# Optimization experiments

Measured on AMD Instinct MI355X. Metric: run time of the kernel, lower is better.

The kernel has to match this reference:

```python
import jax, jax.numpy as jnp
import numpy as np

B, S, D_IN, D_OUT = 4, 4096, 256, 256

def setup_inputs() -> dict:
    key = jax.random.key(0)
    ks = jax.random.split(key, 7)
    scale = 1.0 / np.sqrt(D_IN)
    return {
        "x": jax.random.normal(ks[0], (B, S, D_IN), dtype=jnp.float32),
        "Wq": jax.random.uniform(ks[1], (D_IN, D_OUT), jnp.float32, -scale, scale),
        "bq": jax.random.uniform(ks[2], (D_OUT,), jnp.float32, -scale, scale),
        "Wk": jax.random.uniform(ks[3], (D_IN, D_OUT), jnp.float32, -scale, scale),
        "bk": jax.random.uniform(ks[4], (D_OUT,), jnp.float32, -scale, scale),
        "Wv": jax.random.uniform(ks[5], (D_IN, D_OUT), jnp.float32, -scale, scale),
        "bv": jax.random.uniform(ks[6], (D_OUT,), jnp.float32, -scale, scale),
    }

def reference(x, Wq, bq, Wk, bk, Wv, bv):
    # QKV projections: [B, S, D_OUT]
    q = jnp.einsum("bsd,de->bse", x, Wq) + bq
    k = jnp.einsum("bsd,de->bse", x, Wk) + bk
    v = jnp.einsum("bsd,de->bse", x, Wv) + bv
    # Scaled dot-product attention; full [B, S, S] scores as in the original.
    scores = jnp.einsum("bqe,bke->bqk", q, k) / jnp.sqrt(jnp.asarray(q.shape[-1], q.dtype))
    attn = jax.nn.softmax(scores, axis=-1)
    return jnp.einsum("bqk,bke->bqe", attn, v)
```

## Files before the change

kernel.cpp:

```cpp
#include <hip/hip_runtime.h>
#include <stdint.h>

typedef unsigned short u16;
typedef __attribute__((ext_vector_type(4))) float f32x4;
typedef __attribute__((ext_vector_type(8))) short bf16x8;
typedef __attribute__((ext_vector_type(4))) int i32x4;
typedef __attribute__((ext_vector_type(2))) unsigned int u32x2;

#define SEQ 4096
#define DIM 256
#define QSCALE 0.09016844f

__device__ __forceinline__ u16 f2bf(float f) {
  union { float f; uint32_t u; } v; v.f = f;
  uint32_t r = (v.u + 0x7FFFu + ((v.u >> 16) & 1u)) >> 16;
  return (u16)r;
}

__device__ __forceinline__ void gload_lds16(const void* g, void* lds) {
  __builtin_amdgcn_global_load_lds(
      (const __attribute__((address_space(1))) uint32_t*)g,
      (__attribute__((address_space(3))) uint32_t*)lds, 16, 0, 0);
}

__global__ __launch_bounds__(256) void wt_kernel(const float* __restrict__ Wq,
                                                 const float* __restrict__ Wk,
                                                 const float* __restrict__ Wv,
                                                 u16* __restrict__ wt) {
  int b = blockIdx.x;
  int w = b >> 8;
  int n = b & 255;
  const float* W = (w == 0) ? Wq : ((w == 1) ? Wk : Wv);
  float scale = (w == 0) ? QSCALE : 1.0f;
  int k = threadIdx.x;
  wt[(w * 256 + n) * 256 + k] = f2bf(W[k * 256 + n] * scale);
}

__global__ __launch_bounds__(256) void qkv_kernel(
    const float* __restrict__ x, const float* __restrict__ bq,
    const float* __restrict__ bk, const float* __restrict__ bv,
    const u16* __restrict__ wt, u16* __restrict__ qs, u16* __restrict__ kk,
    char* __restrict__ vt) {
  __shared__ __align__(16) u16 lds_b[16384];
  __shared__ __align__(16) u16 lds_v[4096];
  int tid = threadIdx.x;
  int w = tid >> 6, l = tid & 63;
  int a = l & 15, g = l >> 4;
  int rowbase = blockIdx.x * 64;

  bf16x8 afr[8];
  {
    int row = rowbase + w * 16 + a;
    const float* xr = x + (size_t)row * 256;
#pragma unroll
    for (int ks = 0; ks < 8; ++ks) {
      int k0 = ks * 32 + g * 8;
      union { bf16x8 s; u16 u[8]; } fr;
#pragma unroll
      for (int i = 0; i < 8; ++i) fr.u[i] = f2bf(xr[k0 + i]);
      afr[ks] = fr.s;
    }
  }

  for (int w3 = 0; w3 < 3; ++w3) {
    const float* bias = (w3 == 0) ? bq : ((w3 == 1) ? bk : bv);
    for (int qn = 0; qn < 4; ++qn) {
      {
        const u16* src = wt + (w3 * 256 + qn * 64) * 256;
        for (int j = 0; j < 8; ++j) {
          uint32_t inst = w * 8 + j;
          uint32_t flat = inst * 1024 + l * 16;
          uint32_t row = flat >> 9;
          uint32_t c5 = (flat >> 4) & 31;
          uint32_t sc = (c5 & ~7u) | ((c5 ^ row) & 7u);
          gload_lds16(src + row * 256 + sc * 8, ((char*)lds_b) + inst * 1024);
        }
      }
      __syncthreads();
      f32x4 acc[4];
#pragma unroll
      for (int n0 = 0; n0 < 4; ++n0) acc[n0] = (f32x4){0.f, 0.f, 0.f, 0.f};
#pragma unroll
      for (int ks = 0; ks < 8; ++ks) {
#pragma unroll
        for (int n0 = 0; n0 < 4; ++n0) {
          uint32_t row = n0 * 16 + a;
          uint32_t c5 = ks * 4 + g;
          uint32_t sc = (c5 & ~7u) | ((c5 ^ row) & 7u);
          bf16x8 bfr = *(const bf16x8*)((const char*)lds_b + row * 512 + sc * 16);
          acc[n0] = __builtin_amdgcn_mfma_f32_16x16x32_bf16(afr[ks], bfr, acc[n0], 0, 0, 0);
        }
      }
      if (w3 < 2) {
        u16* out = (w3 == 0) ? qs : kk;
        float bscale = (w3 == 0) ? QSCALE : 1.0f;
#pragma unroll
        for (int n0 = 0; n0 < 4; ++n0) {
          int col = qn * 64 + n0 * 16 + a;
          float bb = bias[col] * bscale;
#pragma unroll
          for (int r = 0; r < 4; ++r) {
            int row = rowbase + w * 16 + g * 4 + r;
            out[(size_t)row * 256 + col] = f2bf(acc[n0][r] + bb);
          }
        }
      } else {
#pragma unroll
        for (int n0 = 0; n0 < 4; ++n0) {
          int col = qn * 64 + n0 * 16 + a;
          float bb = bias[col];
          int dl = n0 * 16 + a;
#pragma unroll
          for (int r = 0; r < 4; ++r) {
            int m = w * 16 + g * 4 + r;
            uint32_t byteoff =
                (uint32_t)dl * 128 + ((((uint32_t)m >> 3) ^ ((uint32_t)dl & 7)) << 4) + (m & 7) * 2;
            *(u16*)((char*)lds_v + byteoff) = f2bf(acc[n0][r] + bb);
          }
        }
        __syncthreads();
        {
          int dl = tid >> 2;
          size_t base = (size_t)blockIdx.x * 32768 + (size_t)(qn * 64 + dl) * 128;
#pragma unroll
          for (int cc = 0; cc < 2; ++cc) {
            uint32_t c = (tid & 3) + cc * 4;
            i32x4 vd = *(const i32x4*)((const char*)lds_v + dl * 128 + ((c ^ (dl & 7)) << 4));
            *(i32x4*)(vt + base + c * 16) = vd;
          }
        }
      }
      __syncthreads();
    }
  }
}

__device__ __forceinline__ void stage4(const char* src, char* ldsbase,
                                       const uint32_t* so, int w) {
#pragma unroll
  for (int j = 0; j < 4; ++j)
    gload_lds16(src + so[j], ldsbase + (w * 4 + j) * 1024);
}

#define PV_STEP(SLOT)                                                          \
  {                                                                            \
    bf16x8 pfr[2][2];                                                          \
    _Pragma("unroll") for (int mt = 0; mt < 2; ++mt)                           \
    _Pragma("unroll") for (int j2 = 0; j2 < 2; ++j2)                           \
        pfr[mt][j2] = *(const bf16x8*)(lds + (SLOT) * 16384 + pro[j2] + mt * 2048); \
    __builtin_amdgcn_s_setprio(1);                                             \
    _Pragma("unroll") for (int mt = 0; mt < 2; ++mt)                           \
    _Pragma("unroll") for (int j2 = 0; j2 < 2; ++j2)                           \
        lacc[mt] = __builtin_amdgcn_mfma_f32_16x16x32_bf16(pfr[mt][j2], ones,  \
                                                           lacc[mt], 0, 0, 0); \
    _Pragma("unroll") for (int d0 = 0; d0 < 8; ++d0)                           \
    _Pragma("unroll") for (int j2 = 0; j2 < 2; ++j2) {                         \
      bf16x8 vfr = *(const bf16x8*)(lds + 65536 + (SLOT) * 32768 + vro[j2] +   \
                                    d0 * 2048);                                \
      o[0][d0] = __builtin_amdgcn_mfma_f32_16x16x32_bf16(pfr[0][j2], vfr, o[0][d0], 0, 0, 0); \
      o[1][d0] = __builtin_amdgcn_mfma_f32_16x16x32_bf16(pfr[1][j2], vfr, o[1][d0], 0, 0, 0); \
    }                                                                          \
    __builtin_amdgcn_s_setprio(0);                                             \
  }

#define TILE(CUR, DO_PV, DO_K)                                                 \
  {                                                                            \
    asm volatile("s_waitcnt vmcnt(0) lgkmcnt(0)" ::: "memory");                \
    __builtin_amdgcn_s_barrier();                                              \
    __builtin_amdgcn_sched_barrier(0);                                         \
    stage4(vstp, lds + 65536 + (CUR) * 32768, vso, w);   \
    if (DO_K) stage4(kstp, lds + ((CUR) ^ 1) * 32768, kso, w);  \
    kstp += 32768;                                                             \
    vstp += 32768;                                                             \
    f32x4 sc[2][2];                                                            \
    _Pragma("unroll") for (int mt = 0; mt < 2; ++mt)                           \
    _Pragma("unroll") for (int n = 0; n < 2; ++n)                              \
        sc[mt][n] = (f32x4){0.f, 0.f, 0.f, 0.f};                               \
    __builtin_amdgcn_s_setprio(1);                                             \
    _Pragma("unroll") for (int n = 0; n < 2; ++n)                              \
    _Pragma("unroll") for (int j = 0; j < 8; ++j) {                            \
      bf16x8 kfr = *(const bf16x8*)(lds + (CUR) * 32768 + kro[j] + n * 8192);  \
      sc[0][n] = __builtin_amdgcn_mfma_f32_16x16x32_bf16(kfr, qfr[0][j], sc[0][n], 0, 0, 0); \
      sc[1][n] = __builtin_amdgcn_mfma_f32_16x16x32_bf16(kfr, qfr[1][j], sc[1][n], 0, 0, 0); \
    }                                                                          \
    __builtin_amdgcn_s_setprio(0);                                             \
    _Pragma("unroll") for (int mt = 0; mt < 2; ++mt)                           \
    _Pragma("unroll") for (int n = 0; n < 2; ++n) {                            \
      float e0 = exp2f(fminf(sc[mt][n][0], 43.f));                             \
      float e1 = exp2f(fminf(sc[mt][n][1], 43.f));                             \
      float e2 = exp2f(fminf(sc[mt][n][2], 43.f));                             \
      float e3 = exp2f(fminf(sc[mt][n][3], 43.f));                             \
      uint32_t p0 = (uint32_t)f2bf(e0) | ((uint32_t)f2bf(e1) << 16);           \
      uint32_t p1 = (uint32_t)f2bf(e2) | ((uint32_t)f2bf(e3) << 16);           \
      u32x2 pk = {p0, p1};                                                     \
      *(u32x2*)(lds + (CUR) * 16384 + pwo[n] + mt * 2048) = pk;                \
    }                                                                          \
    if (DO_PV) PV_STEP((CUR) ^ 1)                                              \
  }

__global__ __launch_bounds__(512, 1) void attn_kernel(
    const u16* __restrict__ qs, const u16* __restrict__ kk,
    const char* __restrict__ vt, float* __restrict__ out,
    float* __restrict__ pOB, float* __restrict__ pl, int split) {
  __shared__ __align__(16) char lds[163840];
  int tid = threadIdx.x;
  int w = tid >> 6, l = tid & 63;
  int a = l & 15, g = l >> 4;
  int qq = w >> 1, sub = w & 1;
  int bx = blockIdx.x;
  int h, batch, qt;
  if (split == 2) { h = bx & 1; batch = (bx >> 1) & 3; qt = bx >> 3; }
  else            { h = 0;      batch = (bx >> 1) & 3; qt = ((bx >> 3) << 1) | (bx & 1); }
  int ntHalf = (split == 2) ? 16 : 32;

  uint32_t a7 = a & 7;
  uint32_t kro[8], vro[2], pro[2], pwo[2], kso[4], vso[4];
#pragma unroll
  for (int j = 0; j < 8; ++j) {
    uint32_t c5 = j * 4 + g;
    kro[j] = (uint32_t)(sub * 32 + a) * 512 +
             (((c5 & ~7u) | ((c5 ^ a7) & 7u)) << 4);
  }
#pragma unroll
  for (int j2 = 0; j2 < 2; ++j2)
    vro[j2] = (uint32_t)(sub * 128 + a) * 128 +
              ((((uint32_t)(j2 * 4 + g)) ^ a7) << 4);
#pragma unroll
  for (int j2 = 0; j2 < 2; ++j2)
    pro[j2] = 131072u + (uint32_t)(qq * 32 + a) * 128 +
              ((((uint32_t)(j2 * 4 + g)) ^ a7) << 4);
#pragma unroll
  for (int n = 0; n < 2; ++n)
    pwo[n] = 131072u + (uint32_t)(qq * 32 + a) * 128 +
             ((((uint32_t)(sub * 4 + n * 2 + (g >> 1))) ^ a7) << 4) + (g & 1) * 8;
#pragma unroll
  for (int j = 0; j < 4; ++j) {
    uint32_t inst = w * 4 + j, flat = inst * 1024 + l * 16;
    {
      uint32_t row = flat >> 9, c5 = (flat >> 4) & 31;
      kso[j] = row * 512 + (((c5 & ~7u) | ((c5 ^ row) & 7u)) << 4);
    }
    {
      uint32_t row = flat >> 7, c3 = (flat >> 4) & 7;
      vso[j] = row * 128 + ((c3 ^ (row & 7)) << 4);
    }
  }

  bf16x8 qfr[2][8];
  {
    const char* qp = (const char*)qs + (size_t)(batch * SEQ + qt * 128) * 512;
#pragma unroll
    for (int mt = 0; mt < 2; ++mt)
#pragma unroll
      for (int j = 0; j < 8; ++j)
        qfr[mt][j] = *(const bf16x8*)(qp + (size_t)(qq * 32 + mt * 16 + a) * 512 +
                                      j * 64 + g * 16);
  }

  f32x4 o[2][8];
  f32x4 lacc[2];
#pragma unroll
  for (int mt = 0; mt < 2; ++mt) {
    lacc[mt] = (f32x4){0.f, 0.f, 0.f, 0.f};
#pragma unroll
    for (int d0 = 0; d0 < 8; ++d0) o[mt][d0] = (f32x4){0.f, 0.f, 0.f, 0.f};
  }
  const short ob = (short)0x3F80;
  bf16x8 ones = {ob, ob, ob, ob, ob, ob, ob, ob};

  const char* kstp = (const char*)kk + (size_t)batch * SEQ * 512 + (size_t)h * 2048 * 512;
  const char* vstp = vt + (size_t)batch * 64 * 32768 + (size_t)h * 32 * 32768;

  stage4(kstp, lds, kso, w);
  kstp += 32768;

  TILE(0, false, true)
  for (int tp = 0; tp < ntHalf - 1; ++tp) {
    TILE(1, true, true)
    TILE(0, true, true)
  }
  TILE(1, true, false)

  asm volatile("s_waitcnt vmcnt(0) lgkmcnt(0)" ::: "memory");
  __builtin_amdgcn_s_barrier();
  __builtin_amdgcn_sched_barrier(0);
  PV_STEP(1)

  float* po = (h == 0) ? out : pOB;
  size_t obase = (size_t)(batch * SEQ + qt * 128 + qq * 32) * 256 + sub * 128;
#pragma unroll
  for (int mt = 0; mt < 2; ++mt)
#pragma unroll
    for (int r = 0; r < 4; ++r) {
#pragma unroll
      for (int d0 = 0; d0 < 8; ++d0)
        po[obase + (size_t)(mt * 16 + g * 4 + r) * 256 + d0 * 16 + a] = o[mt][d0][r];
    }
  if (a == 0 && sub == 0) {
#pragma unroll
    for (int mt = 0; mt < 2; ++mt)
#pragma unroll
      for (int r = 0; r < 4; ++r)
        pl[h * 16384 + (batch * 32 + qt) * 128 + qq * 32 + mt * 16 + g * 4 + r] =
            lacc[mt][r];
  }
}

__global__ __launch_bounds__(256) void combine_kernel(float* __restrict__ out,
                                                      const float* __restrict__ pOB,
                                                      const float* __restrict__ pl,
                                                      int split) {
  int b = blockIdx.x;
  int tid = threadIdx.x;
  int batch = b >> 12;
  int rem = b & 4095;
  int qt = rem >> 7, ql = rem & 127;
  size_t idx = (size_t)b * 256 + tid;
  int li = (batch * 32 + qt) * 128 + ql;
  float lA = pl[li];
  float v;
  if (split == 2) {
    float lB = pl[16384 + li];
    v = (out[idx] + pOB[idx]) / (lA + lB);
  } else {
    v = out[idx] / lA;
  }
  out[idx] = v;
}

extern "C" void kernel_launch(void* const* d_in, const int* in_sizes, int n_in,
                              void* d_out, int out_size, void* d_ws, size_t ws_size,
                              hipStream_t stream) {
  const float* x = (const float*)d_in[0];
  const float* Wq = (const float*)d_in[1];
  const float* bq = (const float*)d_in[2];
  const float* Wk = (const float*)d_in[3];
  const float* bk = (const float*)d_in[4];
  const float* Wv = (const float*)d_in[5];
  const float* bv = (const float*)d_in[6];
  char* ws = (char*)d_ws;
  u16* wt = (u16*)ws;
  u16* qs = (u16*)(ws + 0x60000);
  u16* kk = (u16*)(ws + 0x860000);
  char* vt = ws + 0x1060000;
  float* pl = (float*)(ws + 0x1860000);
  float* pOB = (float*)(ws + 0x1880000);
  int split = (ws_size >= 0x2880000ull) ? 2 : 1;
  wt_kernel<<<dim3(768), dim3(256), 0, stream>>>(Wq, Wk, Wv, wt);
  qkv_kernel<<<dim3(256), dim3(256), 0, stream>>>(x, bq, bk, bv, wt, qs, kk, vt);
  attn_kernel<<<dim3(split * 128), dim3(512), 0, stream>>>(qs, kk, vt, (float*)d_out,
                                                           pOB, pl, split);
  combine_kernel<<<dim3(16384), dim3(256), 0, stream>>>((float*)d_out, pOB, pl, split);
}
```

Measured before the change: 129.1 us.

## Add 4-way key-split attention kernel with single-buffered LDS staging

Adds an attn4_kernel that splits the key dimension into four chunks, launching 512 blocks instead of 256 so more CUs are busy. Each block handles 1024 keys in 16 tiles and writes partial outputs and row sums to workspace. The combine kernel now sums up to four partials. The new kernel drops the double-buffered K/V prefetch and waits on each load, and it adds extra partial-output traffic. It is only used when the workspace is large enough.

```diff
diff --git a/kernel.cpp b/kernel.cpp
--- a/kernel.cpp
+++ b/kernel.cpp
@@ -168,8 +168,8 @@
     asm volatile("s_waitcnt vmcnt(0) lgkmcnt(0)" ::: "memory");                \
     __builtin_amdgcn_s_barrier();                                              \
     __builtin_amdgcn_sched_barrier(0);                                         \
-    stage4(vstp, lds + 65536 + (CUR) * 32768, vso, w);   \
-    if (DO_K) stage4(kstp, lds + ((CUR) ^ 1) * 32768, kso, w);  \
+    stage4(vstp, lds + 65536 + (CUR) * 32768, vso, w);                         \
+    if (DO_K) stage4(kstp, lds + ((CUR) ^ 1) * 32768, kso, w);                 \
     kstp += 32768;                                                             \
     vstp += 32768;                                                             \
     f32x4 sc[2][2];                                                            \
@@ -306,6 +306,169 @@
   }
 }
 
+__global__ __launch_bounds__(512, 4) void attn4_kernel(
+    const u16* __restrict__ qs, const u16* __restrict__ kk,
+    const char* __restrict__ vt, float* __restrict__ out,
+    float* __restrict__ pOB, float* __restrict__ pl) {
+  __shared__ __align__(16) char lds[81920];
+  int tid = threadIdx.x;
+  int w = tid >> 6, l = tid & 63;
+  int a = l & 15, g = l >> 4;
+  int qq = w >> 1, sub = w & 1;
+  int bx = blockIdx.x;
+  int xcd = bx & 7, slot = bx >> 3;
+  int combo = xcd * 2 + (slot >> 5);
+  int batch = combo >> 2, h = combo & 3;
+  int qt = slot & 31;
+
+  uint32_t a7 = a & 7;
+  uint32_t kro[8], vro[2], pro[2], pwo[2], kso[4], vso[4];
+#pragma unroll
+  for (int j = 0; j < 8; ++j) {
+    uint32_t c5 = j * 4 + g;
+    kro[j] = (uint32_t)(sub * 32 + a) * 512 +
+             (((c5 & ~7u) | ((c5 ^ a7) & 7u)) << 4);
+  }
+#pragma unroll
+  for (int j2 = 0; j2 < 2; ++j2)
+    vro[j2] = 32768u + (uint32_t)(sub * 128 + a) * 128 +
+              ((((uint32_t)(j2 * 4 + g)) ^ a7) << 4);
+#pragma unroll
+  for (int j2 = 0; j2 < 2; ++j2)
+    pro[j2] = 65536u + (uint32_t)(qq * 32 + a) * 128 +
+              ((((uint32_t)(j2 * 4 + g)) ^ a7) << 4);
+#pragma unroll
+  for (int n = 0; n < 2; ++n)
+    pwo[n] = 65536u + (uint32_t)(qq * 32 + a) * 128 +
+             ((((uint32_t)(sub * 4 + n * 2 + (g >> 1))) ^ a7) << 4) + (g & 1) * 8;
+#pragma unroll
+  for (int j = 0; j < 4; ++j) {
+    uint32_t inst = w * 4 + j, flat = inst * 1024 + l * 16;
+    {
+      uint32_t row = flat >> 9, c5 = (flat >> 4) & 31;
+      kso[j] = row * 512 + (((c5 & ~7u) | ((c5 ^ row) & 7u)) << 4);
+    }
+    {
+      uint32_t row = flat >> 7, c3 = (flat >> 4) & 7;
+      vso[j] = row * 128 + ((c3 ^ (row & 7)) << 4);
+    }
+  }
+
+  bf16x8 qfr[2][8];
+  {
+    const char* qp = (const char*)qs + (size_t)(batch * SEQ + qt * 128) * 512;
+#pragma unroll
+    for (int mt = 0; mt < 2; ++mt)
+#pragma unroll
+      for (int j = 0; j < 8; ++j)
+        qfr[mt][j] = *(const bf16x8*)(qp + (size_t)(qq * 32 + mt * 16 + a) * 512 +
+                                      j * 64 + g * 16);
+  }
+
+  f32x4 o[2][8];
+  f32x4 lacc[2];
+#pragma unroll
+  for (int mt = 0; mt < 2; ++mt) {
+    lacc[mt] = (f32x4){0.f, 0.f, 0.f, 0.f};
+#pragma unroll
+    for (int d0 = 0; d0 < 8; ++d0) o[mt][d0] = (f32x4){0.f, 0.f, 0.f, 0.f};
+  }
+  const short ob = (short)0x3F80;
+  bf16x8 ones = {ob, ob, ob, ob, ob, ob, ob, ob};
+
+  const char* kstp = (const char*)kk + (size_t)batch * SEQ * 512 + (size_t)h * 1024 * 512;
+  const char* vstp = vt + (size_t)batch * 64 * 32768 + (size_t)h * 16 * 32768;
+
+  for (int t = 0; t < 16; ++t) {
+    stage4(kstp, lds, kso, w);
+    stage4(vstp, lds + 32768, vso, w);
+    kstp += 32768;
+    vstp += 32768;
+    asm volatile("s_waitcnt vmcnt(0)" ::: "memory");
+    __builtin_amdgcn_s_barrier();
+    __builtin_amdgcn_sched_barrier(0);
+
+    f32x4 sc[2][2];
+#pragma unroll
+    for (int mt = 0; mt < 2; ++mt)
+#pragma unroll
+      for (int n = 0; n < 2; ++n) sc[mt][n] = (f32x4){0.f, 0.f, 0.f, 0.f};
+    __builtin_amdgcn_s_setprio(1);
+#pragma unroll
+    for (int n = 0; n < 2; ++n)
+#pragma unroll
+      for (int j = 0; j < 8; ++j) {
+        bf16x8 kfr = *(const bf16x8*)(lds + kro[j] + n * 8192);
+        sc[0][n] = __builtin_amdgcn_mfma_f32_16x16x32_bf16(kfr, qfr[0][j], sc[0][n], 0, 0, 0);
+        sc[1][n] = __builtin_amdgcn_mfma_f32_16x16x32_bf16(kfr, qfr[1][j], sc[1][n], 0, 0, 0);
+      }
+    __builtin_amdgcn_s_setprio(0);
+
+#pragma unroll
+    for (int mt = 0; mt < 2; ++mt)
+#pragma unroll
+      for (int n = 0; n < 2; ++n) {
+        float e0 = exp2f(fminf(sc[mt][n][0], 43.f));
+        float e1 = exp2f(fminf(sc[mt][n][1], 43.f));
+        float e2 = exp2f(fminf(sc[mt][n][2], 43.f));
+        float e3 = exp2f(fminf(sc[mt][n][3], 43.f));
+        uint32_t p0 = (uint32_t)f2bf(e0) | ((uint32_t)f2bf(e1) << 16);
+        uint32_t p1 = (uint32_t)f2bf(e2) | ((uint32_t)f2bf(e3) << 16);
+        u32x2 pk = {p0, p1};
+        *(u32x2*)(lds + pwo[n] + mt * 2048) = pk;
+      }
+    asm volatile("s_waitcnt lgkmcnt(0)" ::: "memory");
+    __builtin_amdgcn_s_barrier();
+    __builtin_amdgcn_sched_barrier(0);
+
+    {
+      bf16x8 pfr[2][2];
+#pragma unroll
+      for (int mt = 0; mt < 2; ++mt)
+#pragma unroll
+        for (int j2 = 0; j2 < 2; ++j2)
+          pfr[mt][j2] = *(const bf16x8*)(lds + pro[j2] + mt * 2048);
+      __builtin_amdgcn_s_setprio(1);
+#pragma unroll
+      for (int mt = 0; mt < 2; ++mt)
+#pragma unroll
+        for (int j2 = 0; j2 < 2; ++j2)
+          lacc[mt] = __builtin_amdgcn_mfma_f32_16x16x32_bf16(pfr[mt][j2], ones,
+                                                             lacc[mt], 0, 0, 0);
+#pragma unroll
+      for (int d0 = 0; d0 < 8; ++d0)
+#pragma unroll
+        for (int j2 = 0; j2 < 2; ++j2) {
+          bf16x8 vfr = *(const bf16x8*)(lds + vro[j2] + d0 * 2048);
+          o[0][d0] = __builtin_amdgcn_mfma_f32_16x16x32_bf16(pfr[0][j2], vfr, o[0][d0], 0, 0, 0);
+          o[1][d0] = __builtin_amdgcn_mfma_f32_16x16x32_bf16(pfr[1][j2], vfr, o[1][d0], 0, 0, 0);
+        }
+      __builtin_amdgcn_s_setprio(0);
+    }
+    __builtin_amdgcn_s_barrier();
+    __builtin_amdgcn_sched_barrier(0);
+  }
+
+  float* po = (h == 0) ? out : (pOB + (size_t)(h - 1) * 0x400000);
+  size_t obase = (size_t)(batch * SEQ + qt * 128 + qq * 32) * 256 + sub * 128;
+#pragma unroll
+  for (int mt = 0; mt < 2; ++mt)
+#pragma unroll
+    for (int r = 0; r < 4; ++r) {
+#pragma unroll
+      for (int d0 = 0; d0 < 8; ++d0)
+        po[obase + (size_t)(mt * 16 + g * 4 + r) * 256 + d0 * 16 + a] = o[mt][d0][r];
+    }
+  if (a == 0 && sub == 0) {
+#pragma unroll
+    for (int mt = 0; mt < 2; ++mt)
+#pragma unroll
+      for (int r = 0; r < 4; ++r)
+        pl[h * 16384 + (batch * 32 + qt) * 128 + qq * 32 + mt * 16 + g * 4 + r] =
+            lacc[mt][r];
+  }
+}
+
 __global__ __launch_bounds__(256) void combine_kernel(float* __restrict__ out,
                                                       const float* __restrict__ pOB,
                                                       const float* __restrict__ pl,
@@ -317,15 +480,14 @@
   int qt = rem >> 7, ql = rem & 127;
   size_t idx = (size_t)b * 256 + tid;
   int li = (batch * 32 + qt) * 128 + ql;
-  float lA = pl[li];
-  float v;
-  if (split == 2) {
-    float lB = pl[16384 + li];
-    v = (out[idx] + pOB[idx]) / (lA + lB);
-  } else {
-    v = out[idx] / lA;
-  }
-  out[idx] = v;
+  float lsum = pl[li];
+  float v = out[idx];
+  if (split >= 2) { lsum += pl[16384 + li]; v += pOB[idx]; }
+  if (split == 4) {
+    lsum += pl[32768 + li] + pl[49152 + li];
+    v += pOB[idx + 0x400000] + pOB[idx + 0x800000];
+  }
+  out[idx] = v / lsum;
 }
 
 extern "C" void kernel_launch(void* const* d_in, const int* in_sizes, int n_in,
@@ -344,11 +506,21 @@
   u16* kk = (u16*)(ws + 0x860000);
   char* vt = ws + 0x1060000;
   float* pl = (float*)(ws + 0x1860000);
-  float* pOB = (float*)(ws + 0x1880000);
-  int split = (ws_size >= 0x2880000ull) ? 2 : 1;
+  float* pOB2 = (float*)(ws + 0x1880000);
+  float* pOB4 = (float*)(ws + 0x18A0000);
+  int split;
+  if (ws_size >= 0x48A0000ull) split = 4;
+  else if (ws_size >= 0x2880000ull) split = 2;
+  else split = 1;
   wt_kernel<<<dim3(768), dim3(256), 0, stream>>>(Wq, Wk, Wv, wt);
   qkv_kernel<<<dim3(256), dim3(256), 0, stream>>>(x, bq, bk, bv, wt, qs, kk, vt);
-  attn_kernel<<<dim3(split * 128), dim3(512), 0, stream>>>(qs, kk, vt, (float*)d_out,
-                                                           pOB, pl, split);
-  combine_kernel<<<dim3(16384), dim3(256), 0, stream>>>((float*)d_out, pOB, pl, split);
-}
+  if (split == 4) {
+    attn4_kernel<<<dim3(512), dim3(512), 0, stream>>>(qs, kk, vt, (float*)d_out,
+                                                      pOB4, pl);
+    combine_kernel<<<dim3(16384), dim3(256), 0, stream>>>((float*)d_out, pOB4, pl, 4);
+  } else {
+    attn_kernel<<<dim3(split * 128), dim3(512), 0, stream>>>(qs, kk, vt, (float*)d_out,
+                                                             pOB2, pl, split);
+    combine_kernel<<<dim3(16384), dim3(256), 0, stream>>>((float*)d_out, pOB2, pl, split);
+  }
+}
```

Result: slower. 477.2 us (+269.6%).

## Use FP8 Q/K for scores, enlarge query tile to 256, split KV four ways

Applied to the files above, without the earlier changes.

Q and K projections are now stored as FP8 (with Q scaled by 4x the softmax factor and K by 0.25 so the range fits FP8), and QK^T uses the fp8 MFMA, halving K staging bytes and LDS footprint. Each attention block now handles 256 query rows instead of 128, which raises reuse of each staged K/V tile, and the KV sequence is split across 4 blocks instead of 2, with XCD-aware block mapping. The combine kernel sums four partial outputs and denominators. FP8 scores reduce accuracy, and the larger register tile (o[4][8]) raises register pressure.

```diff
diff --git a/kernel.cpp b/kernel.cpp
--- a/kernel.cpp
+++ b/kernel.cpp
@@ -2,6 +2,7 @@
 #include <stdint.h>
 
 typedef unsigned short u16;
+typedef long long i64;
 typedef __attribute__((ext_vector_type(4))) float f32x4;
 typedef __attribute__((ext_vector_type(8))) short bf16x8;
 typedef __attribute__((ext_vector_type(4))) int i32x4;
@@ -10,6 +11,7 @@
 #define SEQ 4096
 #define DIM 256
 #define QSCALE 0.09016844f
+#define QS4 0.36067376f
 
 __device__ __forceinline__ u16 f2bf(float f) {
   union { float f; uint32_t u; } v; v.f = f;
@@ -17,10 +19,18 @@
   return (u16)r;
 }
 
+__device__ __forceinline__ uint8_t f2fp8(float f) {
+  return (uint8_t)__builtin_amdgcn_cvt_pk_fp8_f32(f, 0.f, 0, false);
+}
+
 __device__ __forceinline__ void gload_lds16(const void* g, void* lds) {
   __builtin_amdgcn_global_load_lds(
       (const __attribute__((address_space(1))) uint32_t*)g,
       (__attribute__((address_space(3))) uint32_t*)lds, 16, 0, 0);
+}
+
+__device__ __forceinline__ f32x4 mfma8(i64 a, i64 b, f32x4 c) {
+  return __builtin_amdgcn_mfma_f32_16x16x32_fp8_fp8(a, b, c, 0, 0, 0);
 }
 
 __global__ __launch_bounds__(256) void wt_kernel(const float* __restrict__ Wq,
@@ -31,7 +41,7 @@
   int w = b >> 8;
   int n = b & 255;
   const float* W = (w == 0) ? Wq : ((w == 1) ? Wk : Wv);
-  float scale = (w == 0) ? QSCALE : 1.0f;
+  float scale = (w == 0) ? QS4 : ((w == 1) ? 0.25f : 1.0f);
   int k = threadIdx.x;
   wt[(w * 256 + n) * 256 + k] = f2bf(W[k * 256 + n] * scale);
 }
@@ -39,8 +49,8 @@
 __global__ __launch_bounds__(256) void qkv_kernel(
     const float* __restrict__ x, const float* __restrict__ bq,
     const float* __restrict__ bk, const float* __restrict__ bv,
-    const u16* __restrict__ wt, u16* __restrict__ qs, u16* __restrict__ kk,
-    char* __restrict__ vt) {
+    const u16* __restrict__ wt, uint8_t* __restrict__ qs,
+    uint8_t* __restrict__ kk, char* __restrict__ vt) {
   __shared__ __align__(16) u16 lds_b[16384];
   __shared__ __align__(16) u16 lds_v[4096];
   int tid = threadIdx.x;
@@ -92,8 +102,8 @@
         }
       }
       if (w3 < 2) {
-        u16* out = (w3 == 0) ? qs : kk;
-        float bscale = (w3 == 0) ? QSCALE : 1.0f;
+        uint8_t* out8 = (w3 == 0) ? qs : kk;
+        float bscale = (w3 == 0) ? QS4 : 0.25f;
 #pragma unroll
         for (int n0 = 0; n0 < 4; ++n0) {
           int col = qn * 64 + n0 * 16 + a;
@@ -101,7 +111,7 @@
 #pragma unroll
           for (int r = 0; r < 4; ++r) {
             int row = rowbase + w * 16 + g * 4 + r;
-            out[(size_t)row * 256 + col] = f2bf(acc[n0][r] + bb);
+            out8[(size_t)row * 256 + col] = f2fp8(acc[n0][r] + bb);
           }
         }
       } else {
@@ -135,30 +145,28 @@
   }
 }
 
-__device__ __forceinline__ void stage4(const char* src, char* ldsbase,
-                                       const uint32_t* so, int w) {
-#pragma unroll
-  for (int j = 0; j < 4; ++j)
-    gload_lds16(src + so[j], ldsbase + (w * 4 + j) * 1024);
-}
+#define PVB 98304u
+#define VVB 32768u
 
 #define PV_STEP(SLOT)                                                          \
   {                                                                            \
-    bf16x8 pfr[2][2];                                                          \
-    _Pragma("unroll") for (int mt = 0; mt < 2; ++mt)                           \
+    bf16x8 pfr[4][2];                                                          \
+    _Pragma("unroll") for (int mt = 0; mt < 4; ++mt)                           \
     _Pragma("unroll") for (int j2 = 0; j2 < 2; ++j2)                           \
-        pfr[mt][j2] = *(const bf16x8*)(lds + (SLOT) * 16384 + pro[j2] + mt * 2048); \
+        pfr[mt][j2] = *(const bf16x8*)(lds + PVB + (SLOT) * 32768 + pro[j2] +  \
+                                       mt * 2048);                             \
     __builtin_amdgcn_s_setprio(1);                                             \
-    _Pragma("unroll") for (int mt = 0; mt < 2; ++mt)                           \
+    _Pragma("unroll") for (int mt = 0; mt < 4; ++mt)                           \
     _Pragma("unroll") for (int j2 = 0; j2 < 2; ++j2)                           \
         lacc[mt] = __builtin_amdgcn_mfma_f32_16x16x32_bf16(pfr[mt][j2], ones,  \
                                                            lacc[mt], 0, 0, 0); \
     _Pragma("unroll") for (int d0 = 0; d0 < 8; ++d0)                           \
     _Pragma("unroll") for (int j2 = 0; j2 < 2; ++j2) {                         \
-      bf16x8 vfr = *(const bf16x8*)(lds + 65536 + (SLOT) * 32768 + vro[j2] +   \
+      bf16x8 vfr = *(const bf16x8*)(lds + VVB + (SLOT) * 32768 + vro[j2] +     \
                                     d0 * 2048);                                \
-      o[0][d0] = __builtin_amdgcn_mfma_f32_16x16x32_bf16(pfr[0][j2], vfr, o[0][d0], 0, 0, 0); \
-      o[1][d0] = __builtin_amdgcn_mfma_f32_16x16x32_bf16(pfr[1][j2], vfr, o[1][d0], 0, 0, 0); \
+      _Pragma("unroll") for (int mt = 0; mt < 4; ++mt)                         \
+          o[mt][d0] = __builtin_amdgcn_mfma_f32_16x16x32_bf16(                 \
+              pfr[mt][j2], vfr, o[mt][d0], 0, 0, 0);                           \
     }                                                                          \
     __builtin_amdgcn_s_setprio(0);                                             \
   }
@@ -168,23 +176,27 @@
     asm volatile("s_waitcnt vmcnt(0) lgkmcnt(0)" ::: "memory");                \
     __builtin_amdgcn_s_barrier();                                              \
     __builtin_amdgcn_sched_barrier(0);                                         \
-    stage4(vstp, lds + 65536 + (CUR) * 32768, vso, w);   \
-    if (DO_K) stage4(kstp, lds + ((CUR) ^ 1) * 32768, kso, w);  \
-    kstp += 32768;                                                             \
+    _Pragma("unroll") for (int j = 0; j < 4; ++j)                              \
+        gload_lds16(vstp + vso[j], lds + VVB + (CUR) * 32768 + (w * 4 + j) * 1024); \
+    if (DO_K) {                                                                \
+      gload_lds16(kstp + kso[0], lds + ((CUR) ^ 1) * 16384 + (w * 2 + 0) * 1024); \
+      gload_lds16(kstp + kso[1], lds + ((CUR) ^ 1) * 16384 + (w * 2 + 1) * 1024); \
+    }                                                                          \
+    kstp += 16384;                                                             \
     vstp += 32768;                                                             \
-    f32x4 sc[2][2];                                                            \
-    _Pragma("unroll") for (int mt = 0; mt < 2; ++mt)                           \
+    f32x4 sc[4][2];                                                            \
+    _Pragma("unroll") for (int mt = 0; mt < 4; ++mt)                           \
     _Pragma("unroll") for (int n = 0; n < 2; ++n)                              \
         sc[mt][n] = (f32x4){0.f, 0.f, 0.f, 0.f};                               \
     __builtin_amdgcn_s_setprio(1);                                             \
     _Pragma("unroll") for (int n = 0; n < 2; ++n)                              \
     _Pragma("unroll") for (int j = 0; j < 8; ++j) {                            \
-      bf16x8 kfr = *(const bf16x8*)(lds + (CUR) * 32768 + kro[j] + n * 8192);  \
-      sc[0][n] = __builtin_amdgcn_mfma_f32_16x16x32_bf16(kfr, qfr[0][j], sc[0][n], 0, 0, 0); \
-      sc[1][n] = __builtin_amdgcn_mfma_f32_16x16x32_bf16(kfr, qfr[1][j], sc[1][n], 0, 0, 0); \
+      i64 kfr = *(const i64*)(lds + (CUR) * 16384 + kro[j] + n * 4096);        \
+      _Pragma("unroll") for (int mt = 0; mt < 4; ++mt)                         \
+          sc[mt][n] = mfma8(kfr, qfr[mt][j], sc[mt][n]);                       \
     }                                                                          \
     __builtin_amdgcn_s_setprio(0);                                             \
-    _Pragma("unroll") for (int mt = 0; mt < 2; ++mt)                           \
+    _Pragma("unroll") for (int mt = 0; mt < 4; ++mt)                           \
     _Pragma("unroll") for (int n = 0; n < 2; ++n) {                            \
       float e0 = exp2f(fminf(sc[mt][n][0], 43.f));                             \
       float e1 = exp2f(fminf(sc[mt][n][1], 43.f));                             \
@@ -193,13 +205,13 @@
       uint32_t p0 = (uint32_t)f2bf(e0) | ((uint32_t)f2bf(e1) << 16);           \
       uint32_t p1 = (uint32_t)f2bf(e2) | ((uint32_t)f2bf(e3) << 16);           \
       u32x2 pk = {p0, p1};                                                     \
-      *(u32x2*)(lds + (CUR) * 16384 + pwo[n] + mt * 2048) = pk;                \
+      *(u32x2*)(lds + PVB + (CUR) * 32768 + pwo[n] + mt * 2048) = pk;          \
     }                                                                          \
     if (DO_PV) PV_STEP((CUR) ^ 1)                                              \
   }
 
 __global__ __launch_bounds__(512, 1) void attn_kernel(
-    const u16* __restrict__ qs, const u16* __restrict__ kk,
+    const uint8_t* __restrict__ qs, const uint8_t* __restrict__ kk,
     const char* __restrict__ vt, float* __restrict__ out,
     float* __restrict__ pOB, float* __restrict__ pl, int split) {
   __shared__ __align__(16) char lds[163840];
@@ -209,58 +221,67 @@
   int qq = w >> 1, sub = w & 1;
   int bx = blockIdx.x;
   int h, batch, qt;
-  if (split == 2) { h = bx & 1; batch = (bx >> 1) & 3; qt = bx >> 3; }
-  else            { h = 0;      batch = (bx >> 1) & 3; qt = ((bx >> 3) << 1) | (bx & 1); }
-  int ntHalf = (split == 2) ? 16 : 32;
+  if (split == 4) {
+    int xcd = bx & 7, slot = bx >> 3;
+    int combo = xcd * 2 + (slot >> 4);
+    batch = combo >> 2; h = combo & 3; qt = slot & 15;
+  } else {
+    batch = bx >> 4; h = 0; qt = bx & 15;
+  }
+  int nt = (split == 4) ? 16 : 64;
 
   uint32_t a7 = a & 7;
-  uint32_t kro[8], vro[2], pro[2], pwo[2], kso[4], vso[4];
-#pragma unroll
-  for (int j = 0; j < 8; ++j) {
-    uint32_t c5 = j * 4 + g;
-    kro[j] = (uint32_t)(sub * 32 + a) * 512 +
-             (((c5 & ~7u) | ((c5 ^ a7) & 7u)) << 4);
+  uint32_t kro[8], vro[2], pro[2], pwo[2], kso[2], vso[4];
+  {
+    uint32_t row = (uint32_t)(sub * 32 + a);
+#pragma unroll
+    for (int j = 0; j < 8; ++j) {
+      uint32_t c4 = j * 2 + (g >> 1);
+      kro[j] = row * 256 + (((c4 & ~7u) | ((c4 ^ a7) & 7u)) << 4) + (g & 1) * 8;
+    }
   }
 #pragma unroll
   for (int j2 = 0; j2 < 2; ++j2)
     vro[j2] = (uint32_t)(sub * 128 + a) * 128 +
               ((((uint32_t)(j2 * 4 + g)) ^ a7) << 4);
-#pragma unroll
-  for (int j2 = 0; j2 < 2; ++j2)
-    pro[j2] = 131072u + (uint32_t)(qq * 32 + a) * 128 +
-              ((((uint32_t)(j2 * 4 + g)) ^ a7) << 4);
-#pragma unroll
-  for (int n = 0; n < 2; ++n)
-    pwo[n] = 131072u + (uint32_t)(qq * 32 + a) * 128 +
-             ((((uint32_t)(sub * 4 + n * 2 + (g >> 1))) ^ a7) << 4) + (g & 1) * 8;
+  {
+    uint32_t q = (uint32_t)(qq * 64 + a);
+#pragma unroll
+    for (int j2 = 0; j2 < 2; ++j2)
+      pro[j2] = q * 128 + ((((uint32_t)(j2 * 4 + g)) ^ a7) << 4);
+#pragma unroll
+    for (int n = 0; n < 2; ++n)
+      pwo[n] = q * 128 +
+               ((((uint32_t)(sub * 4 + n * 2 + (g >> 1))) ^ a7) << 4) + (g & 1) * 8;
+  }
+#pragma unroll
+  for (int j = 0; j < 2; ++j) {
+    uint32_t inst = w * 2 + j, flat = inst * 1024 + l * 16;
+    uint32_t row = flat >> 8, c4 = (flat >> 4) & 15;
+    kso[j] = row * 256 + (((c4 & ~7u) | ((c4 ^ (row & 7u)) & 7u)) << 4);
+  }
 #pragma unroll
   for (int j = 0; j < 4; ++j) {
     uint32_t inst = w * 4 + j, flat = inst * 1024 + l * 16;
-    {
-      uint32_t row = flat >> 9, c5 = (flat >> 4) & 31;
-      kso[j] = row * 512 + (((c5 & ~7u) | ((c5 ^ row) & 7u)) << 4);
-    }
-    {
-      uint32_t row = flat >> 7, c3 = (flat >> 4) & 7;
-      vso[j] = row * 128 + ((c3 ^ (row & 7)) << 4);
-    }
-  }
-
-  bf16x8 qfr[2][8];
+    uint32_t row = flat >> 7, c3 = (flat >> 4) & 7;
+    vso[j] = row * 128 + ((c3 ^ (row & 7)) << 4);
+  }
+
+  i64 qfr[4][8];
   {
-    const char* qp = (const char*)qs + (size_t)(batch * SEQ + qt * 128) * 512;
-#pragma unroll
-    for (int mt = 0; mt < 2; ++mt)
+    const uint8_t* qp = qs + (size_t)(batch * SEQ + qt * 256) * 256;
+#pragma unroll
+    for (int mt = 0; mt < 4; ++mt)
 #pragma unroll
       for (int j = 0; j < 8; ++j)
-        qfr[mt][j] = *(const bf16x8*)(qp + (size_t)(qq * 32 + mt * 16 + a) * 512 +
-                                      j * 64 + g * 16);
-  }
-
-  f32x4 o[2][8];
-  f32x4 lacc[2];
-#pragma unroll
-  for (int mt = 0; mt < 2; ++mt) {
+        qfr[mt][j] = *(const i64*)(qp + (size_t)(qq * 64 + mt * 16 + a) * 256 +
+                                   j * 32 + g * 8);
+  }
+
+  f32x4 o[4][8];
+  f32x4 lacc[4];
+#pragma unroll
+  for (int mt = 0; mt < 4; ++mt) {
     lacc[mt] = (f32x4){0.f, 0.f, 0.f, 0.f};
 #pragma unroll
     for (int d0 = 0; d0 < 8; ++d0) o[mt][d0] = (f32x4){0.f, 0.f, 0.f, 0.f};
@@ -268,12 +289,14 @@
   const short ob = (short)0x3F80;
   bf16x8 ones = {ob, ob, ob, ob, ob, ob, ob, ob};
 
-  const char* kstp = (const char*)kk + (size_t)batch * SEQ * 512 + (size_t)h * 2048 * 512;
-  const char* vstp = vt + (size_t)batch * 64 * 32768 + (size_t)h * 32 * 32768;
-
-  stage4(kstp, lds, kso, w);
-  kstp += 32768;
-
+  const uint8_t* kstp = kk + (size_t)batch * SEQ * 256 + (size_t)h * 1024 * 256;
+  const char* vstp = vt + (size_t)batch * 64 * 32768 + (size_t)h * 16 * 32768;
+
+  gload_lds16(kstp + kso[0], lds + (w * 2 + 0) * 1024);
+  gload_lds16(kstp + kso[1], lds + (w * 2 + 1) * 1024);
+  kstp += 16384;
+
+  int ntHalf = nt >> 1;
   TILE(0, false, true)
   for (int tp = 0; tp < ntHalf - 1; ++tp) {
     TILE(1, true, true)
@@ -286,10 +309,10 @@
   __builtin_amdgcn_sched_barrier(0);
   PV_STEP(1)
 
-  float* po = (h == 0) ? out : pOB;
-  size_t obase = (size_t)(batch * SEQ + qt * 128 + qq * 32) * 256 + sub * 128;
-#pragma unroll
-  for (int mt = 0; mt < 2; ++mt)
+  float* po = (h == 0) ? out : (pOB + (size_t)(h - 1) * 0x400000);
+  size_t obase = (size_t)(batch * SEQ + qt * 256 + qq * 64) * 256 + sub * 128;
+#pragma unroll
+  for (int mt = 0; mt < 4; ++mt)
 #pragma unroll
     for (int r = 0; r < 4; ++r) {
 #pragma unroll
@@ -298,10 +321,10 @@
     }
   if (a == 0 && sub == 0) {
 #pragma unroll
-    for (int mt = 0; mt < 2; ++mt)
+    for (int mt = 0; mt < 4; ++mt)
 #pragma unroll
       for (int r = 0; r < 4; ++r)
-        pl[h * 16384 + (batch * 32 + qt) * 128 + qq * 32 + mt * 16 + g * 4 + r] =
+        pl[h * 16384 + (batch * 16 + qt) * 256 + qq * 64 + mt * 16 + g * 4 + r] =
             lacc[mt][r];
   }
 }
@@ -312,20 +335,14 @@
                                                       int split) {
   int b = blockIdx.x;
   int tid = threadIdx.x;
-  int batch = b >> 12;
-  int rem = b & 4095;
-  int qt = rem >> 7, ql = rem & 127;
   size_t idx = (size_t)b * 256 + tid;
-  int li = (batch * 32 + qt) * 128 + ql;
-  float lA = pl[li];
-  float v;
-  if (split == 2) {
-    float lB = pl[16384 + li];
-    v = (out[idx] + pOB[idx]) / (lA + lB);
-  } else {
-    v = out[idx] / lA;
-  }
-  out[idx] = v;
+  float lsum = pl[b];
+  float v = out[idx];
+  if (split == 4) {
+    lsum += pl[16384 + b] + pl[32768 + b] + pl[49152 + b];
+    v += pOB[idx] + pOB[idx + 0x400000] + pOB[idx + 0x800000];
+  }
+  out[idx] = v / lsum;
 }
 
 extern "C" void kernel_launch(void* const* d_in, const int* in_sizes, int n_in,
@@ -340,15 +357,15 @@
   const float* bv = (const float*)d_in[6];
   char* ws = (char*)d_ws;
   u16* wt = (u16*)ws;
-  u16* qs = (u16*)(ws + 0x60000);
-  u16* kk = (u16*)(ws + 0x860000);
-  char* vt = ws + 0x1060000;
-  float* pl = (float*)(ws + 0x1860000);
-  float* pOB = (float*)(ws + 0x1880000);
-  int split = (ws_size >= 0x2880000ull) ? 2 : 1;
+  uint8_t* qs = (uint8_t*)(ws + 0x60000);
+  uint8_t* kk = (uint8_t*)(ws + 0x460000);
+  char* vt = ws + 0x860000;
+  float* pl = (float*)(ws + 0x1060000);
+  float* pOB = (float*)(ws + 0x10A0000);
+  int split = (ws_size >= 0x40A0000ull) ? 4 : 1;
   wt_kernel<<<dim3(768), dim3(256), 0, stream>>>(Wq, Wk, Wv, wt);
   qkv_kernel<<<dim3(256), dim3(256), 0, stream>>>(x, bq, bk, bv, wt, qs, kk, vt);
-  attn_kernel<<<dim3(split * 128), dim3(512), 0, stream>>>(qs, kk, vt, (float*)d_out,
-                                                           pOB, pl, split);
+  attn_kernel<<<dim3(split * 64), dim3(512), 0, stream>>>(qs, kk, vt, (float*)d_out,
+                                                          pOB, pl, split);
   combine_kernel<<<dim3(16384), dim3(256), 0, stream>>>((float*)d_out, pOB, pl, split);
 }
```

New measurement: 190.4 us. 47.4% more time.
